# Kernel tuning notes

Measured on AMD Instinct MI355X. Metric: run time of the kernel, lower is better.

The kernel has to match this reference:

```python
import jax, jax.numpy as jnp
import numpy as np

N_P = 50000   # number of 'place' nodes
N_A = 50000   # number of 'a_transition' nodes
E = 1600000   # edges per edge type
IN = 128      # input feature dim
OUT = 64      # HANConv out_channels
H = 4         # heads
D = OUT // H  # per-head dim
HID = 64      # decoder hidden
NEG_SLOPE = 0.2  # HANConv leaky_relu slope


def setup_inputs() -> dict:
    key = jax.random.key(0)
    ks = jax.random.split(key, 24)
    def nrm(i, shape, scale=1.0):
        return jax.random.normal(ks[i], shape, dtype=jnp.float32) * scale
    w = lambda i, shape, fan: nrm(i, shape, (1.0 / fan) ** 0.5)
    return {
        "x_place": nrm(0, (N_P, IN)),
        "x_atrans": nrm(1, (N_A, IN)),
        "e_pa_src": jax.random.randint(ks[2], (E,), 0, N_P),
        "e_pa_dst": jax.random.randint(ks[3], (E,), 0, N_A),
        "e_aa_src": jax.random.randint(ks[4], (E,), 0, N_A),
        "e_aa_dst": jax.random.randint(ks[5], (E,), 0, N_A),
        "e_ap_src": jax.random.randint(ks[6], (E,), 0, N_A),
        "e_ap_dst": jax.random.randint(ks[7], (E,), 0, N_P),
        "Wp_place": w(8, (IN, OUT), IN),
        "bp_place": jnp.zeros((OUT,), jnp.float32),
        "Wp_atrans": w(9, (IN, OUT), IN),
        "bp_atrans": jnp.zeros((OUT,), jnp.float32),
        "asrc_pa": w(10, (H, D), D),
        "adst_pa": w(11, (H, D), D),
        "asrc_aa": w(12, (H, D), D),
        "adst_aa": w(13, (H, D), D),
        "asrc_ap": w(14, (H, D), D),
        "adst_ap": w(15, (H, D), D),
        "Wk": w(16, (OUT, OUT), OUT),
        "bk": jnp.zeros((OUT,), jnp.float32),
        "q": w(17, (OUT,), OUT),
        "Wd1": w(18, (OUT, HID), OUT),
        "bd1": jnp.zeros((HID,), jnp.float32),
        "Wd2": w(19, (HID, 1), HID),
        "bd2": jnp.zeros((1,), jnp.float32),
    }


def _edge_conv(h_src, h_dst, a_src, a_dst, src, dst, n_dst):
    """HANConv node-level attention for one edge type.
    h_src: [N_src, H, D], h_dst: [N_dst, H, D]; returns relu-aggregated [n_dst, H*D]."""
    alpha = (h_src * a_src).sum(-1)[src] + (h_dst * a_dst).sum(-1)[dst]  # [E, H]
    alpha = jax.nn.leaky_relu(alpha, NEG_SLOPE)
    amax = jax.ops.segment_max(alpha, dst, num_segments=n_dst)
    amax = jnp.where(jnp.isfinite(amax), amax, 0.0)  # guard empty neighborhoods
    ex = jnp.exp(alpha - amax[dst])
    den = jax.ops.segment_sum(ex, dst, num_segments=n_dst) + 1e-16  # PyG softmax eps
    wgt = ex / den[dst]                           # scatter-softmax per dst node [E, H]
    msg = h_src[src] * wgt[:, :, None]            # [E, H, D]
    out = jax.ops.segment_sum(msg, dst, num_segments=n_dst)
    return jax.nn.relu(out.reshape(n_dst, H * D))


def _semantic(outs, q, Wk, bk):
    """HANConv semantic-level attention over edge-type embeddings."""
    stk = jnp.stack(outs)                                       # [T, N, OUT]
    score = (q * jnp.tanh(stk @ Wk + bk).mean(axis=1)).sum(-1)  # [T]
    attn = jax.nn.softmax(score)
    return jnp.einsum('t,tnc->nc', attn, stk)


def reference(x_place, x_atrans, e_pa_src, e_pa_dst, e_aa_src, e_aa_dst, e_ap_src, e_ap_dst,
              Wp_place, bp_place, Wp_atrans, bp_atrans,
              asrc_pa, adst_pa, asrc_aa, adst_aa, asrc_ap, adst_ap,
              Wk, bk, q, Wd1, bd1, Wd2, bd2):
    # per-node-type projection, split into heads
    h_p = (x_place @ Wp_place + bp_place).reshape(N_P, H, D)
    h_a = (x_atrans @ Wp_atrans + bp_atrans).reshape(N_A, H, D)
    # node-level attention per edge type
    out_pa = _edge_conv(h_p, h_a, asrc_pa, adst_pa, e_pa_src, e_pa_dst, N_A)
    out_aa = _edge_conv(h_a, h_a, asrc_aa, adst_aa, e_aa_src, e_aa_dst, N_A)
    out_ap = _edge_conv(h_a, h_p, asrc_ap, adst_ap, e_ap_src, e_ap_dst, N_P)
    # semantic-level attention per destination node type
    x_a = _semantic([out_pa, out_aa], q, Wk, bk)   # 'a_transition'
    _xp = _semantic([out_ap], q, Wk, bk)           # 'place' (computed by encoder, unused downstream)
    # decoder MLP on 'a_transition' + softmax over nodes (dim=0)
    z = jax.nn.relu(x_a @ Wd1 + bd1) @ Wd2 + bd2   # [N_A, 1]
    return jax.nn.softmax(z, axis=0)
```

## Files before the change

### kernel.cpp

```cpp
#include <hip/hip_runtime.h>
#include <hip/hip_fp16.h>
#include <math.h>

#define NP 50000
#define NA 50000
#define NE 1600000
#define IN_DIM 128
#define OUT_DIM 64

#define NB 391
#define BCAP 4608
#define P1_CHUNK 8192
#define P1_GRID ((NE + P1_CHUNK - 1) / P1_CHUNK)

typedef _Float16 v8h __attribute__((ext_vector_type(8)));
typedef float    v4f __attribute__((ext_vector_type(4)));

__device__ inline float fast_tanh(float x) {
    const float e = __expf(2.f * x);
    return 1.f - 2.f / (e + 1.f);
}

__global__ __launch_bounds__(256) void proj_kernel(
    const float* __restrict__ xA, const float* __restrict__ WA, const float* __restrict__ bA,
    const float* __restrict__ xB, const float* __restrict__ WB, const float* __restrict__ bB,
    const float* __restrict__ a_pa_src, const float* __restrict__ a_pa_dst,
    const float* __restrict__ a_aa_src, const float* __restrict__ a_aa_dst,
    ushort* __restrict__ hA, ushort* __restrict__ hB,
    float* __restrict__ s_p_src_pa, float* __restrict__ s_a_dst_pa,
    float* __restrict__ s_a_src_aa, float* __restrict__ s_a_dst_aa,
    int* __restrict__ gcur, float* __restrict__ sem, float* __restrict__ esum)
{
    const int type = blockIdx.y;
    const float* x = type ? xB : xA;
    const float* W = type ? WB : WA;
    const float* bias = type ? bB : bA;
    ushort* h_out  = type ? hB : hA;
    const float* c0 = type ? a_pa_dst : a_pa_src;
    float*       s0 = type ? s_a_dst_pa : s_p_src_pa;
    const float* c1 = type ? a_aa_src : nullptr;
    float*       s1 = type ? s_a_src_aa : nullptr;
    const float* c2 = type ? a_aa_dst : nullptr;
    float*       s2 = type ? s_a_dst_aa : nullptr;

    if (blockIdx.x == 0 && type == 0) {
        for (int i = threadIdx.x; i < 2 * NB; i += 256) gcur[i] = i * BCAP;
        if (threadIdx.x < 128) sem[threadIdx.x] = 0.f;
        if (threadIdx.x == 0) esum[0] = 0.f;
    }

    __shared__ _Float16 Wt[64][136];
    const int tid = threadIdx.x;
    {
        const float4* W4 = (const float4*)W;
        #pragma unroll
        for (int i = 0; i < 8; ++i) {
            const int f4i = tid + 256 * i;
            const float4 w = W4[f4i];
            const int k = f4i >> 4, c4 = (f4i & 15) * 4;
            Wt[c4 + 0][k] = (_Float16)w.x;
            Wt[c4 + 1][k] = (_Float16)w.y;
            Wt[c4 + 2][k] = (_Float16)w.z;
            Wt[c4 + 3][k] = (_Float16)w.w;
        }
    }
    __syncthreads();

    const int lane = tid & 63;
    const int wid = tid >> 6;
    const int node0 = (blockIdx.x * 4 + wid) * 16;
    if (node0 >= NP) return;
    const int m = lane & 15;
    const int quad = lane >> 4;

    v4f acc[4] = {};
    #pragma unroll
    for (int kc = 0; kc < 4; ++kc) {
        const int k0 = kc * 32 + quad * 8;
        const float4 xa = *(const float4*)(x + (size_t)(node0 + m) * IN_DIM + k0);
        const float4 xb2 = *(const float4*)(x + (size_t)(node0 + m) * IN_DIM + k0 + 4);
        v8h af;
        af[0] = (_Float16)xa.x;  af[1] = (_Float16)xa.y;
        af[2] = (_Float16)xa.z;  af[3] = (_Float16)xa.w;
        af[4] = (_Float16)xb2.x; af[5] = (_Float16)xb2.y;
        af[6] = (_Float16)xb2.z; af[7] = (_Float16)xb2.w;
        #pragma unroll
        for (int cb = 0; cb < 4; ++cb) {
            const v8h bf = *(const v8h*)&Wt[cb * 16 + m][k0];
            acc[cb] = __builtin_amdgcn_mfma_f32_16x16x32_f16(af, bf, acc[cb], 0, 0, 0);
        }
    }

    #pragma unroll
    for (int cb = 0; cb < 4; ++cb) {
        const int c = cb * 16 + m;
        const float bv = bias[c];
        float hv[4];
        #pragma unroll
        for (int r = 0; r < 4; ++r) {
            hv[r] = acc[cb][r] + bv;
            const int node = node0 + quad * 4 + r;
            h_out[(size_t)node * 64 + c] = __half_as_ushort(__float2half_rn(hv[r]));
        }
        #define DO_SCORE(A, S)                                         \
            if (A) {                                                   \
                const float av = (A)[c];                               \
                float v0 = hv[0]*av, v1 = hv[1]*av, v2 = hv[2]*av, v3 = hv[3]*av; \
                for (int msk = 1; msk <= 8; msk <<= 1) {               \
                    v0 += __shfl_xor(v0, msk);                         \
                    v1 += __shfl_xor(v1, msk);                         \
                    v2 += __shfl_xor(v2, msk);                         \
                    v3 += __shfl_xor(v3, msk);                         \
                }                                                      \
                if (m == 0) {                                          \
                    const int nb = node0 + quad * 4;                   \
                    (S)[(nb + 0) * 4 + cb] = v0;                       \
                    (S)[(nb + 1) * 4 + cb] = v1;                       \
                    (S)[(nb + 2) * 4 + cb] = v2;                       \
                    (S)[(nb + 3) * 4 + cb] = v3;                       \
                }                                                      \
            }
        DO_SCORE(c0, s0)
        DO_SCORE(c1, s1)
        DO_SCORE(c2, s2)
        #undef DO_SCORE
    }
}

__global__ __launch_bounds__(256) void partition_kernel(
    const int* __restrict__ srcA, const int* __restrict__ dstA,
    const int* __restrict__ srcB, const int* __restrict__ dstB,
    int* __restrict__ gpart, int* __restrict__ gcur)
{
    const int type = blockIdx.y;
    const int* src = type ? srcB : srcA;
    const int* dst = type ? dstB : dstA;
    const int ebase = blockIdx.x * P1_CHUNK;
    const int ecount = min(P1_CHUNK, NE - ebase);
    const int tid = threadIdx.x;

    __shared__ int hist[NB];
    __shared__ int starts[NB];
    __shared__ int offs2[NB];
    __shared__ int gbase[NB];
    __shared__ int sorted[P1_CHUNK];

    for (int i = tid; i < NB; i += 256) hist[i] = 0;
    __syncthreads();
    for (int i = tid; i < ecount; i += 256)
        atomicAdd(&hist[dst[ebase + i] >> 7], 1);
    __syncthreads();
    if (tid < 64) {
        int carry = 0;
        for (int r = 0; r < 7; ++r) {
            const int idx = r * 64 + tid;
            const int v = (idx < NB) ? hist[idx] : 0;
            int s = v;
            #pragma unroll
            for (int off = 1; off < 64; off <<= 1) {
                const int t = __shfl_up(s, off);
                if (tid >= off) s += t;
            }
            if (idx < NB) { starts[idx] = carry + s - v; offs2[idx] = carry + s - v; }
            carry += __shfl(s, 63);
        }
    }
    __syncthreads();
    for (int i = tid; i < ecount; i += 256) {
        const int d = dst[ebase + i];
        const int s = src[ebase + i];
        const int pos = atomicAdd(&offs2[d >> 7], 1);
        sorted[pos] = ((d & 127) << 16) | s;
    }
    __syncthreads();
    for (int b = tid; b < NB; b += 256) {
        const int cnt = hist[b];
        gbase[b] = cnt ? atomicAdd(&gcur[type * NB + b], cnt) : 0;
    }
    __syncthreads();
    const int wid = tid >> 6, lane = tid & 63;
    for (int b = wid; b < NB; b += 4) {
        const int st = starts[b], cnt = hist[b], gb = gbase[b];
        for (int i = lane; i < cnt; i += 64) gpart[gb + i] = sorted[st + i];
    }
}

__global__ __launch_bounds__(128) void bscan_kernel(
    const int* __restrict__ gcur, int* __restrict__ bstart)
{
    const int w = threadIdx.x >> 6, lane = threadIdx.x & 63;
    int carry = 0;
    for (int r = 0; r < 7; ++r) {
        const int idx = r * 64 + lane;
        const int flat = w * NB + idx;
        const int v = (idx < NB) ? (gcur[flat] - flat * BCAP) : 0;
        int s = v;
        #pragma unroll
        for (int off = 1; off < 64; off <<= 1) {
            const int t = __shfl_up(s, off);
            if (lane >= off) s += t;
        }
        if (idx < NB) bstart[flat] = carry + s - v;
        carry += __shfl(s, 63);
    }
}

__global__ __launch_bounds__(256) void bucket_sort_kernel(
    int* __restrict__ gpart, const int* __restrict__ gcur,
    const int* __restrict__ bstart,
    int* __restrict__ recA, int* __restrict__ offsA,
    int* __restrict__ recB, int* __restrict__ offsB)
{
    const int b = blockIdx.x, type = blockIdx.y;
    int* rec  = type ? recB  : recA;
    int* offs = type ? offsB : offsA;
    const int flat = type * NB + b;
    const int region = flat * BCAP;
    const int cnt = gcur[flat] - region;
    const int bst = bstart[flat];
    const int tid = threadIdx.x;

    __shared__ int hist[128];
    __shared__ int starts[128];
    __shared__ int offs2[128];
    __shared__ int sorted[BCAP];

    if (tid < 128) hist[tid] = 0;
    __syncthreads();
    for (int i = tid; i < cnt; i += 256)
        atomicAdd(&hist[gpart[region + i] >> 16], 1);
    __syncthreads();
    if (tid < 64) {
        int carry = 0;
        for (int r = 0; r < 2; ++r) {
            const int idx = r * 64 + tid;
            const int v = hist[idx];
            int s = v;
            #pragma unroll
            for (int off = 1; off < 64; off <<= 1) {
                const int t = __shfl_up(s, off);
                if (tid >= off) s += t;
            }
            starts[idx] = carry + s - v;
            offs2[idx]  = carry + s - v;
            carry += __shfl(s, 63);
        }
    }
    __syncthreads();
    for (int i = tid; i < cnt; i += 256) {
        const int pk = gpart[region + i];
        const int pos = atomicAdd(&offs2[pk >> 16], 1);
        sorted[pos] = pk & 0xFFFF;
    }
    __syncthreads();
    for (int i = tid; i < cnt; i += 256) rec[bst + i] = sorted[i];
    if (tid < 128) {
        const int n = b * 128 + tid;
        if (n < NA) offs[n] = bst + starts[tid];
    }
    if (b == NB - 1 && tid == 0) offs[NA] = bst + cnt;
}

__global__ __launch_bounds__(256) void gather_kernel(
    const int* __restrict__ offsA, const int* __restrict__ recA,
    const ushort* __restrict__ hA, const float* __restrict__ ssA,
    const float* __restrict__ sdA, float* __restrict__ outA,
    const int* __restrict__ offsB, const int* __restrict__ recB,
    const ushort* __restrict__ hB, const float* __restrict__ ssB,
    const float* __restrict__ sdB, float* __restrict__ outB, int n_dst)
{
    const int type = blockIdx.y;
    const int* offs = type ? offsB : offsA;
    const int* rec  = type ? recB  : recA;
    const ushort* h_src = type ? hB : hA;
    const float* s_src = type ? ssB : ssA;
    const float* s_dst = type ? sdB : sdA;
    float* outbuf = type ? outB : outA;

    const int lane = threadIdx.x & 63;
    const int d = blockIdx.x * 4 + (threadIdx.x >> 6);
    if (d >= n_dst) return;
    const int q = lane & 15;
    const int sub = lane >> 4;
    const int h = q >> 2;
    const float sd = s_dst[d * 4 + h];
    const int beg = offs[d], end = offs[d + 1];

    float4 acc = make_float4(0.f, 0.f, 0.f, 0.f);
    float wacc = 0.f;
    for (int base = beg; base < end; base += 64) {
        const int c64 = min(64, end - base);
        const int sv = (lane < c64) ? rec[base + lane] : 0;
        const int iters = (c64 + 3) >> 2;
        for (int it = 0; it < iters; ++it) {
            const int idx = it * 4 + sub;
            const int s = __shfl(sv, idx);
            if (idx < c64) {
                float alpha = s_src[s * 4 + h] + sd;
                alpha = (alpha > 0.f) ? alpha : 0.2f * alpha;
                const float w = __expf(alpha);
                const uint2 pk = *(const uint2*)(h_src + (size_t)s * 64 + q * 4);
                const float2 f01 = __half22float2(*(const __half2*)&pk.x);
                const float2 f23 = __half22float2(*(const __half2*)&pk.y);
                acc.x = fmaf(f01.x, w, acc.x);
                acc.y = fmaf(f01.y, w, acc.y);
                acc.z = fmaf(f23.x, w, acc.z);
                acc.w = fmaf(f23.y, w, acc.w);
                wacc += w;
            }
        }
    }
    #pragma unroll
    for (int m = 16; m <= 32; m <<= 1) {
        acc.x += __shfl_xor(acc.x, m);
        acc.y += __shfl_xor(acc.y, m);
        acc.z += __shfl_xor(acc.z, m);
        acc.w += __shfl_xor(acc.w, m);
        wacc  += __shfl_xor(wacc, m);
    }
    if (sub == 0) {
        const float inv = 1.f / (wacc + 1e-16f);
        float4 o;
        o.x = fmaxf(acc.x * inv, 0.f);
        o.y = fmaxf(acc.y * inv, 0.f);
        o.z = fmaxf(acc.z * inv, 0.f);
        o.w = fmaxf(acc.w * inv, 0.f);
        *(float4*)(outbuf + (size_t)d * 64 + q * 4) = o;
    }
}

#define SEM_BLOCKS 512
__global__ __launch_bounds__(256) void semantic_kernel(
    const float* __restrict__ out0, const float* __restrict__ out1,
    const float* __restrict__ Wk, const float* __restrict__ bk,
    float* __restrict__ sem, int n)
{
    __shared__ float Wks[64][64];
    __shared__ float rows[2][4][64];
    const int c = threadIdx.x, ty = threadIdx.y;
    const int tid = ty * 64 + c;
    for (int i = tid; i < 4096; i += 256) ((float*)Wks)[i] = Wk[i];
    const float bkc = bk[c];
    const int ntiles = (n + 3) / 4;
    float acc0 = 0.f, acc1 = 0.f;
    int tile = blockIdx.x;
    float n0 = 0.f, n1 = 0.f;
    {
        const int node = tile * 4 + ty;
        if (node < n) { n0 = out0[(size_t)node * 64 + c]; n1 = out1[(size_t)node * 64 + c]; }
    }
    while (tile < ntiles) {
        __syncthreads();
        rows[0][ty][c] = n0; rows[1][ty][c] = n1;
        __syncthreads();
        const int ntile = tile + gridDim.x;
        if (ntile < ntiles) {
            const int node = ntile * 4 + ty;
            n0 = (node < n) ? out0[(size_t)node * 64 + c] : 0.f;
            n1 = (node < n) ? out1[(size_t)node * 64 + c] : 0.f;
        }
        const int node = tile * 4 + ty;
        if (node < n) {
            float a0 = bkc, a1 = bkc;
            #pragma unroll
            for (int k = 0; k < 64; ++k) {
                const float w = Wks[k][c];
                a0 = fmaf(rows[0][ty][k], w, a0);
                a1 = fmaf(rows[1][ty][k], w, a1);
            }
            acc0 += fast_tanh(a0);
            acc1 += fast_tanh(a1);
        }
        tile = ntile;
    }
    __syncthreads();
    rows[0][ty][c] = acc0; rows[1][ty][c] = acc1;
    __syncthreads();
    if (ty == 0) {
        atomicAdd(&sem[c],      rows[0][0][c] + rows[0][1][c] + rows[0][2][c] + rows[0][3][c]);
        atomicAdd(&sem[64 + c], rows[1][0][c] + rows[1][1][c] + rows[1][2][c] + rows[1][3][c]);
    }
}

__global__ __launch_bounds__(256) void decoder_kernel(
    const float* __restrict__ out0, const float* __restrict__ out1,
    const float* __restrict__ sem, const float* __restrict__ qv,
    const float* __restrict__ Wd1, const float* __restrict__ bd1,
    const float* __restrict__ Wd2, const float* __restrict__ bd2,
    float* __restrict__ z, int n)
{
    __shared__ float xr[4][64];
    __shared__ float attn_s[2];
    const int c = threadIdx.x, ty = threadIdx.y;
    const int node = blockIdx.x * 4 + ty;

    if (ty == 0) {
        float v0 = sem[c] * qv[c];
        float v1 = sem[64 + c] * qv[c];
        for (int off = 32; off >= 1; off >>= 1) {
            v0 += __shfl_xor(v0, off);
            v1 += __shfl_xor(v1, off);
        }
        if (c == 0) {
            const float t0 = v0 / (float)NA, t1 = v1 / (float)NA;
            const float m = fmaxf(t0, t1);
            const float e0 = __expf(t0 - m), e1 = __expf(t1 - m);
            const float inv = 1.f / (e0 + e1);
            attn_s[0] = e0 * inv;
            attn_s[1] = e1 * inv;
        }
    }
    __syncthreads();
    const float a0 = attn_s[0], a1 = attn_s[1];
    if (node < n)
        xr[ty][c] = a0 * out0[(size_t)node * 64 + c] + a1 * out1[(size_t)node * 64 + c];
    __syncthreads();
    if (node >= n) return;
    float acc = bd1[c];
    #pragma unroll
    for (int k = 0; k < 64; ++k)
        acc = fmaf(xr[ty][k], Wd1[k * 64 + c], acc);
    float hv = fmaxf(acc, 0.f) * Wd2[c];
    for (int off = 32; off >= 1; off >>= 1) hv += __shfl_xor(hv, off);
    if (c == 0) z[node] = hv + bd2[0];
}

__global__ __launch_bounds__(256) void softmax_exp_kernel(
    const float* __restrict__ z, float* __restrict__ e,
    float* __restrict__ esum, int n)
{
    float part = 0.f;
    for (int i = blockIdx.x * 256 + threadIdx.x; i < n; i += gridDim.x * 256) {
        const float v = __expf(z[i]);
        e[i] = v;
        part += v;
    }
    for (int off = 32; off >= 1; off >>= 1) part += __shfl_xor(part, off);
    __shared__ float red[4];
    if ((threadIdx.x & 63) == 0) red[threadIdx.x >> 6] = part;
    __syncthreads();
    if (threadIdx.x == 0)
        atomicAdd(esum, red[0] + red[1] + red[2] + red[3]);
}

__global__ __launch_bounds__(256) void softmax_final_kernel(
    const float* __restrict__ e, const float* __restrict__ esum,
    float* __restrict__ out, int n)
{
    const int i = blockIdx.x * 256 + threadIdx.x;
    if (i < n) out[i] = e[i] / (*esum);
}

extern "C" void kernel_launch(void* const* d_in, const int* in_sizes, int n_in,
                              void* d_out, int out_size, void* d_ws, size_t ws_size,
                              hipStream_t stream)
{
    const float* x_place  = (const float*)d_in[0];
    const float* x_atrans = (const float*)d_in[1];
    const int* e_pa_src = (const int*)d_in[2];
    const int* e_pa_dst = (const int*)d_in[3];
    const int* e_aa_src = (const int*)d_in[4];
    const int* e_aa_dst = (const int*)d_in[5];
    const float* Wp_place  = (const float*)d_in[8];
    const float* bp_place  = (const float*)d_in[9];
    const float* Wp_atrans = (const float*)d_in[10];
    const float* bp_atrans = (const float*)d_in[11];
    const float* asrc_pa = (const float*)d_in[12];
    const float* adst_pa = (const float*)d_in[13];
    const float* asrc_aa = (const float*)d_in[14];
    const float* adst_aa = (const float*)d_in[15];
    const float* Wk  = (const float*)d_in[18];
    const float* bk  = (const float*)d_in[19];
    const float* q   = (const float*)d_in[20];
    const float* Wd1 = (const float*)d_in[21];
    const float* bd1 = (const float*)d_in[22];
    const float* Wd2 = (const float*)d_in[23];
    const float* bd2 = (const float*)d_in[24];
    float* out = (float*)d_out;

    float* ws = (float*)d_ws;
    size_t off = 0;
    auto alloc = [&](size_t n) {
        float* p = ws + off; off += (n + 3) & ~(size_t)3; return p;
    };

    ushort* h_p       = (ushort*)alloc((size_t)NP * 32);
    ushort* h_a       = (ushort*)alloc((size_t)NA * 32);
    float* s_p_src_pa = alloc((size_t)NP * 4);
    float* s_a_dst_pa = alloc((size_t)NA * 4);
    float* s_a_src_aa = alloc((size_t)NA * 4);
    float* s_a_dst_aa = alloc((size_t)NA * 4);
    float* out_pa     = alloc((size_t)NA * 64);
    float* out_aa     = alloc((size_t)NA * 64);
    int*   offs_pa    = (int*)alloc(NA + 1);
    int*   offs_aa    = (int*)alloc(NA + 1);
    int*   rec_pa     = (int*)alloc(NE);
    int*   rec_aa     = (int*)alloc(NE);
    int*   gcur       = (int*)alloc(2 * NB);
    int*   bstart     = (int*)alloc(2 * NB);
    float* sem        = alloc(128);
    float* esum       = alloc(4);
    float* zbuf       = alloc(NA);
    float* ebuf       = alloc(NA);
    int* gpart = (int*)out_pa;
    (void)ws_size; (void)in_sizes; (void)n_in; (void)out_size;

    proj_kernel<<<dim3((NP + 63) / 64, 2), 256, 0, stream>>>(
        x_place, Wp_place, bp_place,
        x_atrans, Wp_atrans, bp_atrans,
        asrc_pa, adst_pa, asrc_aa, adst_aa,
        h_p, h_a,
        s_p_src_pa, s_a_dst_pa, s_a_src_aa, s_a_dst_aa,
        gcur, sem, esum);

    partition_kernel<<<dim3(P1_GRID, 2), 256, 0, stream>>>(
        e_pa_src, e_pa_dst, e_aa_src, e_aa_dst, gpart, gcur);
    bscan_kernel<<<1, 128, 0, stream>>>(gcur, bstart);
    bucket_sort_kernel<<<dim3(NB, 2), 256, 0, stream>>>(
        gpart, gcur, bstart, rec_pa, offs_pa, rec_aa, offs_aa);

    gather_kernel<<<dim3((NA + 3) / 4, 2), 256, 0, stream>>>(
        offs_pa, rec_pa, h_p, s_p_src_pa, s_a_dst_pa, out_pa,
        offs_aa, rec_aa, h_a, s_a_src_aa, s_a_dst_aa, out_aa, NA);

    dim3 b64x4(64, 4);
    semantic_kernel<<<SEM_BLOCKS, b64x4, 0, stream>>>(out_pa, out_aa, Wk, bk, sem, NA);
    decoder_kernel<<<NA / 4, b64x4, 0, stream>>>(
        out_pa, out_aa, sem, q, Wd1, bd1, Wd2, bd2, zbuf, NA);
    softmax_exp_kernel<<<196, 256, 0, stream>>>(zbuf, ebuf, esum, NA);
    softmax_final_kernel<<<(NA + 255) / 256, 256, 0, stream>>>(ebuf, esum, out, NA);
}
```

Measured before the change: 385.0 us.

## Vectorize partition loads, drop bucket scan kernel, fuse softmax exp into decoder

The partition kernel now reads edge indices as int4 vectors and scatters each sorted element directly to its global slot instead of doing a per-bucket wave copy. The separate bucket-start scan kernel is removed; each bucket_sort block instead sums the preceding bucket counts itself. The decoder becomes a persistent grid that computes the exp of its logits and accumulates the softmax denominator, which removes the separate exp kernel and the z buffer. This saves launches and memory passes, at the cost of redundant prefix work per block and less parallelism in the decoder.

```diff
diff --git a/kernel.cpp b/kernel.cpp
--- a/kernel.cpp
+++ b/kernel.cpp
@@ -44,7 +44,7 @@
     float*       s2 = type ? s_a_dst_aa : nullptr;
 
     if (blockIdx.x == 0 && type == 0) {
-        for (int i = threadIdx.x; i < 2 * NB; i += 256) gcur[i] = i * BCAP;
+        for (int i = threadIdx.x; i < 2 * NB; i += 256) gcur[i] = 0;
         if (threadIdx.x < 128) sem[threadIdx.x] = 0.f;
         if (threadIdx.x == 0) esum[0] = 0.f;
     }
@@ -137,6 +137,7 @@
     const int* dst = type ? dstB : dstA;
     const int ebase = blockIdx.x * P1_CHUNK;
     const int ecount = min(P1_CHUNK, NE - ebase);
+    const int ec4 = ecount >> 2;
     const int tid = threadIdx.x;
 
     __shared__ int hist[NB];
@@ -147,8 +148,16 @@
 
     for (int i = tid; i < NB; i += 256) hist[i] = 0;
     __syncthreads();
-    for (int i = tid; i < ecount; i += 256)
-        atomicAdd(&hist[dst[ebase + i] >> 7], 1);
+    {
+        const int4* d4p = (const int4*)(dst + ebase);
+        for (int i = tid; i < ec4; i += 256) {
+            const int4 d4 = d4p[i];
+            atomicAdd(&hist[d4.x >> 7], 1);
+            atomicAdd(&hist[d4.y >> 7], 1);
+            atomicAdd(&hist[d4.z >> 7], 1);
+            atomicAdd(&hist[d4.w >> 7], 1);
+        }
+    }
     __syncthreads();
     if (tid < 64) {
         int carry = 0;
@@ -166,48 +175,34 @@
         }
     }
     __syncthreads();
-    for (int i = tid; i < ecount; i += 256) {
-        const int d = dst[ebase + i];
-        const int s = src[ebase + i];
-        const int pos = atomicAdd(&offs2[d >> 7], 1);
-        sorted[pos] = ((d & 127) << 16) | s;
+    {
+        const int4* d4p = (const int4*)(dst + ebase);
+        const int4* s4p = (const int4*)(src + ebase);
+        for (int i = tid; i < ec4; i += 256) {
+            const int4 d4 = d4p[i];
+            const int4 s4 = s4p[i];
+            sorted[atomicAdd(&offs2[d4.x >> 7], 1)] = (d4.x << 16) | s4.x;
+            sorted[atomicAdd(&offs2[d4.y >> 7], 1)] = (d4.y << 16) | s4.y;
+            sorted[atomicAdd(&offs2[d4.z >> 7], 1)] = (d4.z << 16) | s4.z;
+            sorted[atomicAdd(&offs2[d4.w >> 7], 1)] = (d4.w << 16) | s4.w;
+        }
     }
     __syncthreads();
     for (int b = tid; b < NB; b += 256) {
         const int cnt = hist[b];
-        gbase[b] = cnt ? atomicAdd(&gcur[type * NB + b], cnt) : 0;
-    }
-    __syncthreads();
-    const int wid = tid >> 6, lane = tid & 63;
-    for (int b = wid; b < NB; b += 4) {
-        const int st = starts[b], cnt = hist[b], gb = gbase[b];
-        for (int i = lane; i < cnt; i += 64) gpart[gb + i] = sorted[st + i];
-    }
-}
-
-__global__ __launch_bounds__(128) void bscan_kernel(
-    const int* __restrict__ gcur, int* __restrict__ bstart)
-{
-    const int w = threadIdx.x >> 6, lane = threadIdx.x & 63;
-    int carry = 0;
-    for (int r = 0; r < 7; ++r) {
-        const int idx = r * 64 + lane;
-        const int flat = w * NB + idx;
-        const int v = (idx < NB) ? (gcur[flat] - flat * BCAP) : 0;
-        int s = v;
-        #pragma unroll
-        for (int off = 1; off < 64; off <<= 1) {
-            const int t = __shfl_up(s, off);
-            if (lane >= off) s += t;
-        }
-        if (idx < NB) bstart[flat] = carry + s - v;
-        carry += __shfl(s, 63);
+        const int flat = type * NB + b;
+        gbase[b] = cnt ? (flat * BCAP + atomicAdd(&gcur[flat], cnt)) : 0;
+    }
+    __syncthreads();
+    for (int i = tid; i < ecount; i += 256) {
+        const int v = sorted[i];
+        const int b = ((unsigned)v) >> 23;
+        gpart[gbase[b] + (i - starts[b])] = v & 0x7FFFFF;
     }
 }
 
 __global__ __launch_bounds__(256) void bucket_sort_kernel(
     int* __restrict__ gpart, const int* __restrict__ gcur,
-    const int* __restrict__ bstart,
     int* __restrict__ recA, int* __restrict__ offsA,
     int* __restrict__ recB, int* __restrict__ offsB)
 {
@@ -216,17 +211,29 @@
     int* offs = type ? offsB : offsA;
     const int flat = type * NB + b;
     const int region = flat * BCAP;
-    const int cnt = gcur[flat] - region;
-    const int bst = bstart[flat];
+    const int cnt = gcur[flat];
     const int tid = threadIdx.x;
 
     __shared__ int hist[128];
     __shared__ int starts[128];
     __shared__ int offs2[128];
     __shared__ int sorted[BCAP];
-
-    if (tid < 128) hist[tid] = 0;
-    __syncthreads();
+    __shared__ int redp[4];
+    __shared__ int s_bst;
+
+    {
+        int part = 0;
+        for (int j = tid; j < b; j += 256) part += gcur[type * NB + j];
+        #pragma unroll
+        for (int off = 32; off >= 1; off >>= 1) part += __shfl_xor(part, off);
+        if ((tid & 63) == 0) redp[tid >> 6] = part;
+        if (tid < 128) hist[tid] = 0;
+        __syncthreads();
+        if (tid == 0) s_bst = redp[0] + redp[1] + redp[2] + redp[3];
+    }
+    __syncthreads();
+    const int bst = s_bst;
+
     for (int i = tid; i < cnt; i += 256)
         atomicAdd(&hist[gpart[region + i] >> 16], 1);
     __syncthreads();
@@ -382,17 +389,18 @@
     }
 }
 
+#define DEC_BLOCKS 256
 __global__ __launch_bounds__(256) void decoder_kernel(
     const float* __restrict__ out0, const float* __restrict__ out1,
     const float* __restrict__ sem, const float* __restrict__ qv,
     const float* __restrict__ Wd1, const float* __restrict__ bd1,
     const float* __restrict__ Wd2, const float* __restrict__ bd2,
-    float* __restrict__ z, int n)
+    float* __restrict__ ebuf, float* __restrict__ esum, int n)
 {
     __shared__ float xr[4][64];
     __shared__ float attn_s[2];
+    __shared__ float redp[4];
     const int c = threadIdx.x, ty = threadIdx.y;
-    const int node = blockIdx.x * 4 + ty;
 
     if (ty == 0) {
         float v0 = sem[c] * qv[c];
@@ -412,35 +420,36 @@
     }
     __syncthreads();
     const float a0 = attn_s[0], a1 = attn_s[1];
-    if (node < n)
-        xr[ty][c] = a0 * out0[(size_t)node * 64 + c] + a1 * out1[(size_t)node * 64 + c];
-    __syncthreads();
-    if (node >= n) return;
-    float acc = bd1[c];
-    #pragma unroll
-    for (int k = 0; k < 64; ++k)
-        acc = fmaf(xr[ty][k], Wd1[k * 64 + c], acc);
-    float hv = fmaxf(acc, 0.f) * Wd2[c];
-    for (int off = 32; off >= 1; off >>= 1) hv += __shfl_xor(hv, off);
-    if (c == 0) z[node] = hv + bd2[0];
-}
-
-__global__ __launch_bounds__(256) void softmax_exp_kernel(
-    const float* __restrict__ z, float* __restrict__ e,
-    float* __restrict__ esum, int n)
-{
-    float part = 0.f;
-    for (int i = blockIdx.x * 256 + threadIdx.x; i < n; i += gridDim.x * 256) {
-        const float v = __expf(z[i]);
-        e[i] = v;
-        part += v;
-    }
-    for (int off = 32; off >= 1; off >>= 1) part += __shfl_xor(part, off);
-    __shared__ float red[4];
-    if ((threadIdx.x & 63) == 0) red[threadIdx.x >> 6] = part;
-    __syncthreads();
-    if (threadIdx.x == 0)
-        atomicAdd(esum, red[0] + red[1] + red[2] + red[3]);
+    const float bd2v = bd2[0];
+    const float wd2c = Wd2[c];
+    const int ntiles = (n + 3) / 4;
+    float epart = 0.f;
+
+    for (int tile = blockIdx.x; tile < ntiles; tile += DEC_BLOCKS) {
+        const int node = tile * 4 + ty;
+        __syncthreads();
+        if (node < n)
+            xr[ty][c] = a0 * out0[(size_t)node * 64 + c] + a1 * out1[(size_t)node * 64 + c];
+        __syncthreads();
+        if (node < n) {
+            float acc = bd1[c];
+            #pragma unroll
+            for (int k = 0; k < 64; ++k)
+                acc = fmaf(xr[ty][k], Wd1[k * 64 + c], acc);
+            float hv = fmaxf(acc, 0.f) * wd2c;
+            for (int off = 32; off >= 1; off >>= 1) hv += __shfl_xor(hv, off);
+            if (c == 0) {
+                const float e = __expf(hv + bd2v);
+                ebuf[node] = e;
+                epart += e;
+            }
+        }
+    }
+    __syncthreads();
+    if (c == 0) redp[ty] = epart;
+    __syncthreads();
+    if (ty == 0 && c == 0)
+        atomicAdd(esum, redp[0] + redp[1] + redp[2] + redp[3]);
 }
 
 __global__ __launch_bounds__(256) void softmax_final_kernel(
@@ -497,10 +506,8 @@
     int*   rec_pa     = (int*)alloc(NE);
     int*   rec_aa     = (int*)alloc(NE);
     int*   gcur       = (int*)alloc(2 * NB);
-    int*   bstart     = (int*)alloc(2 * NB);
     float* sem        = alloc(128);
     float* esum       = alloc(4);
-    float* zbuf       = alloc(NA);
     float* ebuf       = alloc(NA);
     int* gpart = (int*)out_pa;
     (void)ws_size; (void)in_sizes; (void)n_in; (void)out_size;
@@ -515,9 +522,8 @@
 
     partition_kernel<<<dim3(P1_GRID, 2), 256, 0, stream>>>(
         e_pa_src, e_pa_dst, e_aa_src, e_aa_dst, gpart, gcur);
-    bscan_kernel<<<1, 128, 0, stream>>>(gcur, bstart);
     bucket_sort_kernel<<<dim3(NB, 2), 256, 0, stream>>>(
-        gpart, gcur, bstart, rec_pa, offs_pa, rec_aa, offs_aa);
+        gpart, gcur, rec_pa, offs_pa, rec_aa, offs_aa);
 
     gather_kernel<<<dim3((NA + 3) / 4, 2), 256, 0, stream>>>(
         offs_pa, rec_pa, h_p, s_p_src_pa, s_a_dst_pa, out_pa,
@@ -525,8 +531,7 @@
 
     dim3 b64x4(64, 4);
     semantic_kernel<<<SEM_BLOCKS, b64x4, 0, stream>>>(out_pa, out_aa, Wk, bk, sem, NA);
-    decoder_kernel<<<NA / 4, b64x4, 0, stream>>>(
-        out_pa, out_aa, sem, q, Wd1, bd1, Wd2, bd2, zbuf, NA);
-    softmax_exp_kernel<<<196, 256, 0, stream>>>(zbuf, ebuf, esum, NA);
+    decoder_kernel<<<DEC_BLOCKS, b64x4, 0, stream>>>(
+        out_pa, out_aa, sem, q, Wd1, bd1, Wd2, bd2, ebuf, esum, NA);
     softmax_final_kernel<<<(NA + 255) / 256, 256, 0, stream>>>(ebuf, esum, out, NA);
 }
```

Measured after the change: 394.9 us. 2.6% more time.
